# Kernel optimization log

Measured on AMD Instinct MI355X. Metric: run time of the kernel, lower is better.

## Reference

```python
import jax, jax.numpy as jnp
import numpy as np

NODES = [2048, 4096, 8192]
LAMB = 0.5  # sparsity penalty, applied only at layer 0


def tanh_deriv(x):
    t = jnp.tanh(x)
    return 1.0 - t * t


def setup_inputs() -> dict:
    key = jax.random.key(0)
    k1, k2, k3, k4 = jax.random.split(key, 4)
    B = 256
    batch_inp = jax.random.normal(k1, (B, NODES[2]), jnp.float32)
    # torch Linear weight layout: (out_features, in_features)
    W0 = jax.random.normal(k2, (NODES[1], NODES[0]), jnp.float32) / np.float32(np.sqrt(NODES[0]))
    W1 = jax.random.normal(k3, (NODES[2], NODES[1]), jnp.float32) / np.float32(np.sqrt(NODES[1]))
    memory = jax.random.normal(k4, (NODES[0],), jnp.float32) * 0.1
    return {"batch_inp": batch_inp, "W0": W0, "W1": W1, "memory": memory,
            "n_iters": 8, "inf_lr": 0.05}


def reference(batch_inp, W0, W1, memory, n_iters, inf_lr):
    B = batch_inp.shape[0]
    inf_lr = jnp.float32(inf_lr)

    def compute_errs(v0, v1, v2):
        # update_err_nodes: e_l = v_l - pred_l
        e0 = v0 - memory
        e1 = v1 - jnp.tanh(v0) @ W0.T   # [B, n1]
        e2 = v2 - jnp.tanh(v1) @ W1.T   # [B, n2]
        return e0, e1, e2

    def energy(e0, e1, e2):
        return (jnp.sum(e0 * e0) + jnp.sum(e1 * e1) + jnp.sum(e2 * e2)) * (100.0 / B)

    # set_nodes: v0 = memory (broadcast over batch -- identical to torch broadcasting),
    # v1 = forward prediction, v2 clamped to input.
    v0 = jnp.broadcast_to(memory, (B, NODES[0]))
    v1 = jnp.tanh(v0) @ W0.T
    v2 = batch_inp
    e0, e1, e2 = compute_errs(v0, v1, v2)

    def step(carry, _):
        v0, v1, e0, e1, e2 = carry
        # update_val_nodes (torch.no_grad block): all errs are pre-update values
        d0 = -e0 - LAMB * jnp.sign(v0) + tanh_deriv(v0) * (e1 @ W0)
        nv0 = jax.lax.stop_gradient(jax.nn.relu(v0 + inf_lr * d0))
        d1 = -e1 + tanh_deriv(v1) * (e2 @ W1)
        nv1 = jax.lax.stop_gradient(jax.nn.relu(v1 + inf_lr * d1))
        ne0, ne1, ne2 = compute_errs(nv0, nv1, v2)
        return (nv0, nv1, ne0, ne1, ne2), energy(ne0, ne1, ne2)

    _, losses = jax.lax.scan(step, (v0, v1, e0, e1, e2), None, length=n_iters)
    return losses  # [n_iters] per-iteration energies (inf_losses)
```

## Files before the change

kernel.cpp:

```cpp
#include <hip/hip_runtime.h>
#include <hip/hip_bf16.h>
#include <stdint.h>


typedef short short8x __attribute__((ext_vector_type(8)));
typedef float float4x __attribute__((ext_vector_type(4)));
typedef unsigned short u16;
typedef u16 u16x8 __attribute__((ext_vector_type(8)));

static constexpr float LOSS_SCALE = 100.0f / 256.0f;

__device__ __forceinline__ u16 f2b(float x) {
    union { float f; uint32_t u; } v{x};
    uint32_t b = v.u + 0x7fffu + ((v.u >> 16) & 1u);
    return (u16)(b >> 16);
}

__device__ __forceinline__ float signf_(float x) {
    return (x > 0.f) ? 1.f : ((x < 0.f) ? -1.f : 0.f);
}

__device__ __forceinline__ void gload_lds16(const void* g, void* lds) {
    __builtin_amdgcn_global_load_lds(
        (const __attribute__((address_space(1))) void*)g,
        (__attribute__((address_space(3))) void*)lds, 16, 0, 0);
}

__global__ void k_zero(float* p, int n) {
    int i = blockIdx.x * blockDim.x + threadIdx.x;
    if (i < n) p[i] = 0.f;
}

__global__ __launch_bounds__(256) void k_cast_both(
    const float* __restrict__ in, u16* __restrict__ outN, u16* __restrict__ outT,
    int R, int C) {
    __shared__ float tile[32][33];
    int x = blockIdx.x * 32 + threadIdx.x;
#pragma unroll
    for (int k = 0; k < 32; k += 8) {
        int y = blockIdx.y * 32 + threadIdx.y + k;
        float v = in[(size_t)y * C + x];
        tile[threadIdx.y + k][threadIdx.x] = v;
        outN[(size_t)y * C + x] = f2b(v);
    }
    __syncthreads();
    int ox = blockIdx.y * 32 + threadIdx.x;
#pragma unroll
    for (int k = 0; k < 32; k += 8) {
        int oy = blockIdx.x * 32 + threadIdx.y + k;
        outT[(size_t)oy * R + ox] = f2b(tile[threadIdx.x][threadIdx.y + k]);
    }
}

__global__ void k_fill_v0(float* __restrict__ v0, const float* __restrict__ memory,
                          int n, int mask) {
    int i = blockIdx.x * blockDim.x + threadIdx.x;
    if (i < n) v0[i] = memory[i & mask];
}

__global__ void k_tanh(float* __restrict__ dst, const float* __restrict__ src, int n) {
    int i = blockIdx.x * blockDim.x + threadIdx.x;
    if (i < n) dst[i] = tanhf(src[i]);
}

__global__ void k_rowdot(const float* __restrict__ x, const float* __restrict__ W,
                         float* __restrict__ out, int K) {
    int i = blockIdx.x;
    const float* w = W + (size_t)i * K;
    float s = 0.f;
    for (int j = threadIdx.x; j < K; j += 256) s += x[j] * w[j];
    __shared__ float red[256];
    red[threadIdx.x] = s;
    __syncthreads();
    for (int st = 128; st > 0; st >>= 1) {
        if (threadIdx.x < st) red[threadIdx.x] += red[threadIdx.x + st];
        __syncthreads();
    }
    if (threadIdx.x == 0) out[i] = red[0];
}

__global__ void k_bcast_v1_e1(float* __restrict__ v1, float* __restrict__ e1,
                              u16* __restrict__ e1b,
                              const float* __restrict__ r1, int n, int mask) {
    int i = blockIdx.x * blockDim.x + threadIdx.x;
    if (i < n) { v1[i] = r1[i & mask]; e1[i] = 0.f; e1b[i] = 0; }
}

__global__ void k_e2_init(u16* __restrict__ e2b, const float* __restrict__ inp,
                          const float* __restrict__ r2, int n, int mask) {
    int i = blockIdx.x * blockDim.x + threadIdx.x;
    if (i < n) e2b[i] = f2b(inp[i] - r2[i & mask]);
}

struct GGR {
    const u16* A;
    const u16* Bt;
    float* Cp;
    int N, K, nCol, ks;
};

__device__ void gemm_part(const GGR& g, int t, u16* stage) {
    const int tid = threadIdx.x;
    const int w = tid >> 6, l = tid & 63;
    const int lm = l & 15, lq = l >> 4;
    const int cb = t / g.ks, kq = t - cb * g.ks;
    const int K = g.K;
    const int Ksl = K / g.ks;
    const int nCh = Ksl >> 5;
    const int col0 = cb * 64;

    u16* base = stage + (w << 13);
    const u16* aSrc = g.A + (size_t)(w * 64 + (l >> 2)) * K + kq * Ksl + (l & 3) * 8;
    const u16* bSrc = g.Bt + (size_t)(col0 + (l >> 2)) * K + kq * Ksl + (l & 3) * 8;
    const size_t rStep = (size_t)16 * K;

    int aoff[4];
#pragma unroll
    for (int i = 0; i < 4; ++i) aoff[i] = (i * 16 + lm) * 32 + lq * 8;

    float4x acc[4][4];
#pragma unroll
    for (int i = 0; i < 4; ++i)
#pragma unroll
        for (int j = 0; j < 4; ++j) acc[i][j] = (float4x)0.f;

#define ISSUE(c, b) { \
    u16* ab = base + (b) * 4096; \
    const u16* as = aSrc + (c) * 32; \
    const u16* bs = bSrc + (c) * 32; \
    gload_lds16(as, ab);             gload_lds16(as + rStep, ab + 512); \
    gload_lds16(as + 2*rStep, ab + 1024); gload_lds16(as + 3*rStep, ab + 1536); \
    gload_lds16(bs, ab + 2048);      gload_lds16(bs + rStep, ab + 2560); \
    gload_lds16(bs + 2*rStep, ab + 3072); gload_lds16(bs + 3*rStep, ab + 3584); }

#define COMPUTE(b) { \
    u16* ab = base + (b) * 4096; \
    short8x a[4], bb[4]; \
    _Pragma("unroll") for (int i = 0; i < 4; ++i) a[i] = *(const short8x*)(ab + aoff[i]); \
    _Pragma("unroll") for (int j = 0; j < 4; ++j) bb[j] = *(const short8x*)(ab + 2048 + aoff[j]); \
    _Pragma("unroll") for (int i = 0; i < 4; ++i) \
    _Pragma("unroll") for (int j = 0; j < 4; ++j) \
        acc[i][j] = __builtin_amdgcn_mfma_f32_16x16x32_bf16(a[i], bb[j], acc[i][j], 0, 0, 0); }

    ISSUE(0, 0);
    int c = 0;
    for (; c < nCh - 1; ++c) {
        __builtin_amdgcn_sched_barrier(0);
        ISSUE(c + 1, (c + 1) & 1);
        __builtin_amdgcn_sched_barrier(0);
        __builtin_amdgcn_s_waitcnt(0x0F78);
        __builtin_amdgcn_sched_barrier(0);
        COMPUTE(c & 1);
    }
    __builtin_amdgcn_sched_barrier(0);
    __builtin_amdgcn_s_waitcnt(0x0F70);
    __builtin_amdgcn_sched_barrier(0);
    COMPUTE(c & 1);
#undef ISSUE
#undef COMPUTE

    float* cp = g.Cp + ((size_t)(kq * 256 + w * 64) * g.N + col0);
#pragma unroll
    for (int i = 0; i < 4; ++i)
#pragma unroll
        for (int j = 0; j < 4; ++j)
#pragma unroll
            for (int r = 0; r < 4; ++r)
                cp[(size_t)(i * 16 + lq * 4 + r) * g.N + j * 16 + lm] = acc[i][j][r];
}

__global__ __launch_bounds__(256, 2) void pcn_gemm(GGR ga, GGR gb, int nA) {
    __shared__ u16 stage[32768];
    int bx = blockIdx.x;
    if (bx < nA) gemm_part(ga, bx, stage);
    else         gemm_part(gb, bx - nA, stage);
}

struct EGR {
    const float* P;
    const float* x0;
    const float* x1;
    float* y0;
    u16* y0b;
    u16* y1b;
    float* loss;
    const float* lr;
    int N, nCol, ks;
};

template <int EPI>
__device__ void epi_tile(const EGR& g, int tile, float* red8) {
    const int t = threadIdx.x;
    const int w = t >> 6, l = t & 63;
    const int rowBlk = tile / g.nCol, colBlk = tile - rowBlk * g.nCol;
    const int row0 = rowBlk * 64, col0 = colBlk * 64;
    const int row = t >> 3, c8 = (t & 7) * 8;
    const size_t idx = (size_t)(row0 + row) * g.N + col0 + c8;
    const size_t plane = (size_t)256 * g.N;

    const float* p0 = g.P + idx;
    float4x cv[2];
    cv[0] = *(const float4x*)(p0);
    cv[1] = *(const float4x*)(p0 + 4);
    for (int q = 1; q < g.ks; ++q) {
        cv[0] += *(const float4x*)(p0 + (size_t)q * plane);
        cv[1] += *(const float4x*)(p0 + (size_t)q * plane + 4);
    }

    float lr = 0.f;
    if (EPI == 1 || EPI == 2) lr = *g.lr;
    float lsum = 0.f;

    if (EPI == 1) {
        float4x vv[2], mm[2], nv[2]; u16x8 tb;
        vv[0] = *(const float4x*)(g.x0 + idx);       vv[1] = *(const float4x*)(g.x0 + idx + 4);
        mm[0] = *(const float4x*)(g.x1 + col0 + c8); mm[1] = *(const float4x*)(g.x1 + col0 + c8 + 4);
#pragma unroll
        for (int h = 0; h < 2; ++h)
#pragma unroll
            for (int e = 0; e < 4; ++e) {
                float v = vv[h][e], th = tanhf(v), td = 1.f - th * th;
                float d0 = (mm[h][e] - v) - 0.5f * signf_(v) + td * cv[h][e];
                float x = v + lr * d0;
                x = x > 0.f ? x : 0.f;
                nv[h][e] = x;
                tb[h * 4 + e] = f2b(tanhf(x));
                float ne0 = x - mm[h][e];
                lsum += ne0 * ne0;
            }
        *(float4x*)(g.y0 + idx) = nv[0];
        *(float4x*)(g.y0 + idx + 4) = nv[1];
        *(u16x8*)(g.y1b + idx) = tb;
    } else if (EPI == 2) {
        float4x vv[2], ee[2], nv[2]; u16x8 tb;
        vv[0] = *(const float4x*)(g.x0 + idx);     vv[1] = *(const float4x*)(g.x0 + idx + 4);
        ee[0] = *(const float4x*)(g.x1 + idx);     ee[1] = *(const float4x*)(g.x1 + idx + 4);
#pragma unroll
        for (int h = 0; h < 2; ++h)
#pragma unroll
            for (int e = 0; e < 4; ++e) {
                float v = vv[h][e], th = tanhf(v), td = 1.f - th * th;
                float x = v + lr * (-ee[h][e] + td * cv[h][e]);
                x = x > 0.f ? x : 0.f;
                nv[h][e] = x;
                tb[h * 4 + e] = f2b(tanhf(x));
            }
        *(float4x*)(g.y0 + idx) = nv[0];
        *(float4x*)(g.y0 + idx + 4) = nv[1];
        *(u16x8*)(g.y1b + idx) = tb;
    } else if (EPI == 3) {
        float4x vv[2], ne[2]; u16x8 nb;
        vv[0] = *(const float4x*)(g.x0 + idx);     vv[1] = *(const float4x*)(g.x0 + idx + 4);
#pragma unroll
        for (int h = 0; h < 2; ++h)
#pragma unroll
            for (int e = 0; e < 4; ++e) {
                float x = vv[h][e] - cv[h][e];
                ne[h][e] = x;
                nb[h * 4 + e] = f2b(x);
                lsum += x * x;
            }
        *(float4x*)(g.y0 + idx) = ne[0];
        *(float4x*)(g.y0 + idx + 4) = ne[1];
        *(u16x8*)(g.y0b + idx) = nb;
    } else {
        float4x vv[2]; u16x8 nb;
        vv[0] = *(const float4x*)(g.x0 + idx);     vv[1] = *(const float4x*)(g.x0 + idx + 4);
#pragma unroll
        for (int h = 0; h < 2; ++h)
#pragma unroll
            for (int e = 0; e < 4; ++e) {
                float x = vv[h][e] - cv[h][e];
                nb[h * 4 + e] = f2b(x);
                lsum += x * x;
            }
        *(u16x8*)(g.y1b + idx) = nb;
    }

    if (EPI != 2) {
#pragma unroll
        for (int off = 32; off > 0; off >>= 1) lsum += __shfl_down(lsum, off);
        if (l == 0) red8[w] = lsum;
        __syncthreads();
        if (t == 0) {
            float s = 0.f;
#pragma unroll
            for (int q = 0; q < 8; ++q) s += red8[q];
            atomicAdd(g.loss, s * LOSS_SCALE);
        }
    }
}

template <int EPIA, int EPIB>
__global__ __launch_bounds__(512) void pcn_epi(EGR ga, EGR gb, int nA) {
    __shared__ float red8[8];
    int bx = blockIdx.x;
    if (bx < nA) epi_tile<EPIA>(ga, bx, red8);
    else         epi_tile<EPIB>(gb, bx - nA, red8);
}

extern "C" void kernel_launch(void* const* d_in, const int* in_sizes, int n_in,
                              void* d_out, int out_size, void* d_ws, size_t ws_size,
                              hipStream_t stream)
{
    const float* batch_inp = (const float*)d_in[0];
    const float* W0        = (const float*)d_in[1];
    const float* W1        = (const float*)d_in[2];
    const float* memory    = (const float*)d_in[3];
    const float* lr_ptr    = (const float*)d_in[5];
    float* out = (float*)d_out;

    const int n0 = 2048, n1 = 4096, n2 = 8192, Bn = 256;

    char* ws = (char*)d_ws;
    auto alloc_f = [&](size_t n) { float* p = (float*)ws; ws += n * 4; return p; };
    auto alloc_b = [&](size_t n) { u16* p = (u16*)ws; ws += n * 2; return p; };

    float* v0  = alloc_f((size_t)Bn * n0);
    float* v1  = alloc_f((size_t)Bn * n1);
    float* e1  = alloc_f((size_t)Bn * n1);
    u16*   e1b = alloc_b((size_t)Bn * n1);
    u16*   e2b = alloc_b((size_t)Bn * n2);
    u16*   T0b = alloc_b((size_t)Bn * n0);
    u16*   T1b = alloc_b((size_t)Bn * n1);
    u16*   W0b  = alloc_b((size_t)n1 * n0);
    u16*   W0Tb = alloc_b((size_t)n0 * n1);
    u16*   W1b  = alloc_b((size_t)n2 * n1);
    u16*   W1Tb = alloc_b((size_t)n1 * n2);
    float* tm = alloc_f(n0);
    float* r1 = alloc_f(n1);
    float* t1 = alloc_f(n1);
    float* r2 = alloc_f(n2);
    float* CpA = alloc_f((size_t)8 * Bn * n1);
    float* CpB = alloc_f((size_t)4 * Bn * n0);

    k_zero<<<1, 32, 0, stream>>>(out, 8);
    k_cast_both<<<dim3(n0 / 32, n1 / 32), dim3(32, 8), 0, stream>>>(W0, W0b, W0Tb, n1, n0);
    k_cast_both<<<dim3(n1 / 32, n2 / 32), dim3(32, 8), 0, stream>>>(W1, W1b, W1Tb, n2, n1);
    k_fill_v0<<<(Bn * n0) / 256, 256, 0, stream>>>(v0, memory, Bn * n0, n0 - 1);
    k_tanh<<<n0 / 256, 256, 0, stream>>>(tm, memory, n0);
    k_rowdot<<<n1, 256, 0, stream>>>(tm, W0, r1, n0);
    k_tanh<<<n1 / 256, 256, 0, stream>>>(t1, r1, n1);
    k_bcast_v1_e1<<<(Bn * n1) / 256, 256, 0, stream>>>(v1, e1, e1b, r1, Bn * n1, n1 - 1);
    k_rowdot<<<n2, 256, 0, stream>>>(t1, W1, r2, n1);
    k_e2_init<<<(Bn * n2) / 256, 256, 0, stream>>>(e2b, batch_inp, r2, Bn * n2, n2 - 1);

    for (int it = 0; it < 8; ++it) {
        float* loss = out + it;

        GGR g2{e2b, W1Tb, CpA, n1, n2, n1 / 64, 8};
        GGR g1{e1b, W0Tb, CpB, n0, n1, n0 / 64, 4};
        pcn_gemm<<<(n1 / 64) * 8 + (n0 / 64) * 4, 256, 0, stream>>>(g2, g1, (n1 / 64) * 8);

        EGR e2g{CpA, v1, e1, v1, nullptr, T1b, nullptr, lr_ptr, n1, n1 / 64, 8};
        EGR e1g{CpB, v0, memory, v0, nullptr, T0b, loss, lr_ptr, n0, n0 / 64, 4};
        pcn_epi<2, 1><<<4 * (n1 / 64) + 4 * (n0 / 64), 512, 0, stream>>>(
            e2g, e1g, 4 * (n1 / 64));

        GGR g4{T1b, W1b, CpA, n2, n1, n2 / 64, 4};
        GGR g3{T0b, W0b, CpB, n1, n0, n1 / 64, 2};
        pcn_gemm<<<(n2 / 64) * 4 + (n1 / 64) * 2, 256, 0, stream>>>(g4, g3, (n2 / 64) * 4);

        EGR e4g{CpA, batch_inp, nullptr, nullptr, nullptr, e2b, loss, nullptr, n2, n2 / 64, 4};
        EGR e3g{CpB, v1, nullptr, e1, e1b, nullptr, loss, nullptr, n1, n1 / 64, 2};
        pcn_epi<4, 3><<<4 * (n2 / 64) + 4 * (n1 / 64), 512, 0, stream>>>(
            e4g, e3g, 4 * (n2 / 64));
    }
}
```

Baseline: 1.303 ms.

## Single-buffer GEMM staging for higher occupancy, widen split-K, vectorize cast and rowdot

The GEMM drops its double-buffered LDS staging for a single buffer, halving shared memory so launch bounds allow four blocks per CU. Each chunk now issues its loads and waits for them before computing, so in-block prefetch overlap is lost in exchange for more resident waves. When the workspace is large enough, split-K factors and partial-sum planes double, giving more blocks at the cost of more partial traffic in the epilogue. The weight cast/transpose kernel is rewritten with 64x64 bf16 tiles and vector stores, and the row-dot kernel now uses float4 loads.

```diff
diff --git a/kernel.cpp b/kernel.cpp
--- a/kernel.cpp
+++ b/kernel.cpp
@@ -6,6 +6,7 @@
 typedef short short8x __attribute__((ext_vector_type(8)));
 typedef float float4x __attribute__((ext_vector_type(4)));
 typedef unsigned short u16;
+typedef u16 u16x4 __attribute__((ext_vector_type(4)));
 typedef u16 u16x8 __attribute__((ext_vector_type(8)));
 
 static constexpr float LOSS_SCALE = 100.0f / 256.0f;
@@ -34,21 +35,28 @@
 __global__ __launch_bounds__(256) void k_cast_both(
     const float* __restrict__ in, u16* __restrict__ outN, u16* __restrict__ outT,
     int R, int C) {
-    __shared__ float tile[32][33];
-    int x = blockIdx.x * 32 + threadIdx.x;
-#pragma unroll
-    for (int k = 0; k < 32; k += 8) {
-        int y = blockIdx.y * 32 + threadIdx.y + k;
-        float v = in[(size_t)y * C + x];
-        tile[threadIdx.y + k][threadIdx.x] = v;
-        outN[(size_t)y * C + x] = f2b(v);
+    __shared__ u16 tile[64][68];
+    const int t = threadIdx.x;
+    const int c4 = (t & 15) * 4;
+    const int r0 = t >> 4;
+    const int gx = blockIdx.x * 64, gy = blockIdx.y * 64;
+#pragma unroll
+    for (int k = 0; k < 64; k += 16) {
+        int y = r0 + k;
+        float4x v = *(const float4x*)(in + (size_t)(gy + y) * C + gx + c4);
+        u16x4 pk = { f2b(v[0]), f2b(v[1]), f2b(v[2]), f2b(v[3]) };
+        *(u16x4*)(outN + (size_t)(gy + y) * C + gx + c4) = pk;
+        *(u16x4*)(&tile[y][c4]) = pk;
     }
     __syncthreads();
-    int ox = blockIdx.y * 32 + threadIdx.x;
-#pragma unroll
-    for (int k = 0; k < 32; k += 8) {
-        int oy = blockIdx.x * 32 + threadIdx.y + k;
-        outT[(size_t)oy * R + ox] = f2b(tile[threadIdx.x][threadIdx.y + k]);
+    const int w = t >> 6, l = t & 63;
+#pragma unroll
+    for (int rr = 0; rr < 16; rr += 8) {
+        int r = w * 16 + rr;
+        u16x8 pk;
+#pragma unroll
+        for (int k = 0; k < 8; ++k) pk[k] = tile[r + k][l];
+        *(u16x8*)(outT + (size_t)(gx + l) * R + gy + r) = pk;
     }
 }
 
@@ -66,9 +74,13 @@
 __global__ void k_rowdot(const float* __restrict__ x, const float* __restrict__ W,
                          float* __restrict__ out, int K) {
     int i = blockIdx.x;
-    const float* w = W + (size_t)i * K;
+    const float4* w = (const float4*)(W + (size_t)i * K);
+    const float4* xv = (const float4*)x;
     float s = 0.f;
-    for (int j = threadIdx.x; j < K; j += 256) s += x[j] * w[j];
+    for (int j = threadIdx.x; j < (K >> 2); j += 256) {
+        float4 a = xv[j], b = w[j];
+        s += a.x * b.x + a.y * b.y + a.z * b.z + a.w * b.w;
+    }
     __shared__ float red[256];
     red[threadIdx.x] = s;
     __syncthreads();
@@ -109,7 +121,7 @@
     const int nCh = Ksl >> 5;
     const int col0 = cb * 64;
 
-    u16* base = stage + (w << 13);
+    u16* base = stage + (w << 12);
     const u16* aSrc = g.A + (size_t)(w * 64 + (l >> 2)) * K + kq * Ksl + (l & 3) * 8;
     const u16* bSrc = g.Bt + (size_t)(col0 + (l >> 2)) * K + kq * Ksl + (l & 3) * 8;
     const size_t rStep = (size_t)16 * K;
@@ -124,38 +136,30 @@
 #pragma unroll
         for (int j = 0; j < 4; ++j) acc[i][j] = (float4x)0.f;
 
-#define ISSUE(c, b) { \
-    u16* ab = base + (b) * 4096; \
+#define ISSUE(c) { \
     const u16* as = aSrc + (c) * 32; \
     const u16* bs = bSrc + (c) * 32; \
-    gload_lds16(as, ab);             gload_lds16(as + rStep, ab + 512); \
-    gload_lds16(as + 2*rStep, ab + 1024); gload_lds16(as + 3*rStep, ab + 1536); \
-    gload_lds16(bs, ab + 2048);      gload_lds16(bs + rStep, ab + 2560); \
-    gload_lds16(bs + 2*rStep, ab + 3072); gload_lds16(bs + 3*rStep, ab + 3584); }
-
-#define COMPUTE(b) { \
-    u16* ab = base + (b) * 4096; \
+    gload_lds16(as, base);               gload_lds16(as + rStep, base + 512); \
+    gload_lds16(as + 2*rStep, base + 1024); gload_lds16(as + 3*rStep, base + 1536); \
+    gload_lds16(bs, base + 2048);        gload_lds16(bs + rStep, base + 2560); \
+    gload_lds16(bs + 2*rStep, base + 3072); gload_lds16(bs + 3*rStep, base + 3584); }
+
+#define COMPUTE() { \
     short8x a[4], bb[4]; \
-    _Pragma("unroll") for (int i = 0; i < 4; ++i) a[i] = *(const short8x*)(ab + aoff[i]); \
-    _Pragma("unroll") for (int j = 0; j < 4; ++j) bb[j] = *(const short8x*)(ab + 2048 + aoff[j]); \
+    _Pragma("unroll") for (int i = 0; i < 4; ++i) a[i] = *(const short8x*)(base + aoff[i]); \
+    _Pragma("unroll") for (int j = 0; j < 4; ++j) bb[j] = *(const short8x*)(base + 2048 + aoff[j]); \
     _Pragma("unroll") for (int i = 0; i < 4; ++i) \
     _Pragma("unroll") for (int j = 0; j < 4; ++j) \
         acc[i][j] = __builtin_amdgcn_mfma_f32_16x16x32_bf16(a[i], bb[j], acc[i][j], 0, 0, 0); }
 
-    ISSUE(0, 0);
-    int c = 0;
-    for (; c < nCh - 1; ++c) {
+    for (int c = 0; c < nCh; ++c) {
         __builtin_amdgcn_sched_barrier(0);
-        ISSUE(c + 1, (c + 1) & 1);
+        ISSUE(c);
         __builtin_amdgcn_sched_barrier(0);
-        __builtin_amdgcn_s_waitcnt(0x0F78);
+        __builtin_amdgcn_s_waitcnt(0x0F70);
         __builtin_amdgcn_sched_barrier(0);
-        COMPUTE(c & 1);
-    }
-    __builtin_amdgcn_sched_barrier(0);
-    __builtin_amdgcn_s_waitcnt(0x0F70);
-    __builtin_amdgcn_sched_barrier(0);
-    COMPUTE(c & 1);
+        COMPUTE();
+    }
 #undef ISSUE
 #undef COMPUTE
 
@@ -169,8 +173,8 @@
                 cp[(size_t)(i * 16 + lq * 4 + r) * g.N + j * 16 + lm] = acc[i][j][r];
 }
 
-__global__ __launch_bounds__(256, 2) void pcn_gemm(GGR ga, GGR gb, int nA) {
-    __shared__ u16 stage[32768];
+__global__ __launch_bounds__(256, 4) void pcn_gemm(GGR ga, GGR gb, int nA) {
+    __shared__ u16 stage[16384];
     int bx = blockIdx.x;
     if (bx < nA) gemm_part(ga, bx, stage);
     else         gemm_part(gb, bx - nA, stage);
@@ -312,6 +316,14 @@
 
     const int n0 = 2048, n1 = 4096, n2 = 8192, Bn = 256;
 
+    const bool big = ws_size >= (size_t)260 * 1024 * 1024;
+    const int ks2 = big ? 16 : 8;
+    const int ks1 = big ? 8 : 4;
+    const int ks4 = big ? 8 : 4;
+    const int ks3 = big ? 4 : 2;
+    const int planesA = big ? 16 : 8;
+    const int planesB = big ? 8 : 4;
+
     char* ws = (char*)d_ws;
     auto alloc_f = [&](size_t n) { float* p = (float*)ws; ws += n * 4; return p; };
     auto alloc_b = [&](size_t n) { u16* p = (u16*)ws; ws += n * 2; return p; };
@@ -331,12 +343,12 @@
     float* r1 = alloc_f(n1);
     float* t1 = alloc_f(n1);
     float* r2 = alloc_f(n2);
-    float* CpA = alloc_f((size_t)8 * Bn * n1);
-    float* CpB = alloc_f((size_t)4 * Bn * n0);
+    float* CpA = alloc_f((size_t)planesA * Bn * n1);
+    float* CpB = alloc_f((size_t)planesB * Bn * n0);
 
     k_zero<<<1, 32, 0, stream>>>(out, 8);
-    k_cast_both<<<dim3(n0 / 32, n1 / 32), dim3(32, 8), 0, stream>>>(W0, W0b, W0Tb, n1, n0);
-    k_cast_both<<<dim3(n1 / 32, n2 / 32), dim3(32, 8), 0, stream>>>(W1, W1b, W1Tb, n2, n1);
+    k_cast_both<<<dim3(n0 / 64, n1 / 64), 256, 0, stream>>>(W0, W0b, W0Tb, n1, n0);
+    k_cast_both<<<dim3(n1 / 64, n2 / 64), 256, 0, stream>>>(W1, W1b, W1Tb, n2, n1);
     k_fill_v0<<<(Bn * n0) / 256, 256, 0, stream>>>(v0, memory, Bn * n0, n0 - 1);
     k_tanh<<<n0 / 256, 256, 0, stream>>>(tm, memory, n0);
     k_rowdot<<<n1, 256, 0, stream>>>(tm, W0, r1, n0);
@@ -348,21 +360,23 @@
     for (int it = 0; it < 8; ++it) {
         float* loss = out + it;
 
-        GGR g2{e2b, W1Tb, CpA, n1, n2, n1 / 64, 8};
-        GGR g1{e1b, W0Tb, CpB, n0, n1, n0 / 64, 4};
-        pcn_gemm<<<(n1 / 64) * 8 + (n0 / 64) * 4, 256, 0, stream>>>(g2, g1, (n1 / 64) * 8);
-
-        EGR e2g{CpA, v1, e1, v1, nullptr, T1b, nullptr, lr_ptr, n1, n1 / 64, 8};
-        EGR e1g{CpB, v0, memory, v0, nullptr, T0b, loss, lr_ptr, n0, n0 / 64, 4};
+        GGR g2{e2b, W1Tb, CpA, n1, n2, n1 / 64, ks2};
+        GGR g1{e1b, W0Tb, CpB, n0, n1, n0 / 64, ks1};
+        pcn_gemm<<<(n1 / 64) * ks2 + (n0 / 64) * ks1, 256, 0, stream>>>(
+            g2, g1, (n1 / 64) * ks2);
+
+        EGR e2g{CpA, v1, e1, v1, nullptr, T1b, nullptr, lr_ptr, n1, n1 / 64, ks2};
+        EGR e1g{CpB, v0, memory, v0, nullptr, T0b, loss, lr_ptr, n0, n0 / 64, ks1};
         pcn_epi<2, 1><<<4 * (n1 / 64) + 4 * (n0 / 64), 512, 0, stream>>>(
             e2g, e1g, 4 * (n1 / 64));
 
-        GGR g4{T1b, W1b, CpA, n2, n1, n2 / 64, 4};
-        GGR g3{T0b, W0b, CpB, n1, n0, n1 / 64, 2};
-        pcn_gemm<<<(n2 / 64) * 4 + (n1 / 64) * 2, 256, 0, stream>>>(g4, g3, (n2 / 64) * 4);
-
-        EGR e4g{CpA, batch_inp, nullptr, nullptr, nullptr, e2b, loss, nullptr, n2, n2 / 64, 4};
-        EGR e3g{CpB, v1, nullptr, e1, e1b, nullptr, loss, nullptr, n1, n1 / 64, 2};
+        GGR g4{T1b, W1b, CpA, n2, n1, n2 / 64, ks4};
+        GGR g3{T0b, W0b, CpB, n1, n0, n1 / 64, ks3};
+        pcn_gemm<<<(n2 / 64) * ks4 + (n1 / 64) * ks3, 256, 0, stream>>>(
+            g4, g3, (n2 / 64) * ks4);
+
+        EGR e4g{CpA, batch_inp, nullptr, nullptr, nullptr, e2b, loss, nullptr, n2, n2 / 64, ks4};
+        EGR e3g{CpB, v1, nullptr, e1, e1b, nullptr, loss, nullptr, n1, n1 / 64, ks3};
         pcn_epi<4, 3><<<4 * (n2 / 64) + 4 * (n1 / 64), 512, 0, stream>>>(
             e4g, e3g, 4 * (n2 / 64));
     }
```

Measured after the change: 1.593 ms. 22.2% more time.
